# Kernel optimization log

Measured on AMD Instinct MI355X. Metric: run time of the kernel, lower is better.

Reference implementation:

```python
import jax, jax.numpy as jnp
import numpy as np

D_MODEL = 256; N_HEADS = 8; N_LAYERS = 6; D_FF = 1024; BATCH = 1
INPUT_SHAPES = [(24, 24, 24), (12, 12, 12), (6, 6, 6)]
NUM_ORGANS = 20; QPO = 5; LEVELS = 3
NUM_PATCHES = [int(np.prod(s)) for s in INPUT_SHAPES]
S_TOTAL = int(sum(NUM_PATCHES))          # 15768 flattened multi-level patches
NUM_Q = QPO * LEVELS * NUM_ORGANS        # 300 queries


def _build_attn_mask():
    # Same structure as FocusedAttnDecoder.generate_attn_mask: per-organ
    # normalized bbox, scaled (floor/ceil) into each feature level, queries
    # ordered organ-major then level then query copy. True = blocked.
    rng = np.random.RandomState(0)
    mask = np.ones((NUM_Q, S_TOTAL), dtype=bool)
    offsets = np.cumsum([0] + NUM_PATCHES[:-1])
    qi = 0
    for organ in range(NUM_ORGANS):
        lo = rng.uniform(0.0, 0.5, 3)
        hi = np.minimum(lo + rng.uniform(0.15, 0.45, 3), 1.0)
        for lvl in range(LEVELS):
            shp = np.array(INPUT_SHAPES[lvl])
            a = np.floor(lo * shp).astype(int)
            b = np.ceil(hi * shp).astype(int)
            dummy = np.zeros(INPUT_SHAPES[lvl], dtype=bool)
            dummy[a[0]:b[0], a[1]:b[1], a[2]:b[2]] = True
            idx = np.nonzero(dummy.ravel())[0] + offsets[lvl]
            for _ in range(QPO):
                mask[qi, idx] = False
                qi += 1
    return mask


def _xavier(key, shape):
    fan_in, fan_out = shape[-1], shape[-2]
    lim = float(np.sqrt(6.0 / (fan_in + fan_out)))
    return jax.random.uniform(key, shape, minval=-lim, maxval=lim, dtype=jnp.float32)


def setup_inputs() -> dict:
    key = jax.random.key(0)
    ks = jax.random.split(key, 9)
    L, C, F = N_LAYERS, D_MODEL, D_FF
    return {
        "srcs": jax.random.normal(ks[0], (BATCH, C, S_TOTAL), jnp.float32),
        "pos_embeds": jax.random.normal(ks[1], (BATCH, C, S_TOTAL), jnp.float32),
        "query_embed": jax.random.normal(ks[2], (NUM_Q, 2 * C), jnp.float32),
        "attn_mask": jnp.asarray(_build_attn_mask()),
        "sa_in_w": _xavier(ks[3], (L, 3 * C, C)), "sa_in_b": jnp.zeros((L, 3 * C), jnp.float32),
        "sa_out_w": _xavier(ks[4], (L, C, C)), "sa_out_b": jnp.zeros((L, C), jnp.float32),
        "ca_in_w": _xavier(ks[5], (L, 3 * C, C)), "ca_in_b": jnp.zeros((L, 3 * C), jnp.float32),
        "ca_out_w": _xavier(ks[6], (L, C, C)), "ca_out_b": jnp.zeros((L, C), jnp.float32),
        "ln1_w": jnp.ones((L, C), jnp.float32), "ln1_b": jnp.zeros((L, C), jnp.float32),
        "ln2_w": jnp.ones((L, C), jnp.float32), "ln2_b": jnp.zeros((L, C), jnp.float32),
        "ln3_w": jnp.ones((L, C), jnp.float32), "ln3_b": jnp.zeros((L, C), jnp.float32),
        "ff1_w": _xavier(ks[7], (L, F, C)), "ff1_b": jnp.zeros((L, F), jnp.float32),
        "ff2_w": _xavier(ks[8], (L, C, F)), "ff2_b": jnp.zeros((L, C), jnp.float32),
    }


def _ln(x, w, b, eps=1e-5):
    m = jnp.mean(x, axis=-1, keepdims=True)
    v = jnp.mean(jnp.square(x - m), axis=-1, keepdims=True)
    return (x - m) * jax.lax.rsqrt(v + eps) * w + b


def _mha(q_in, k_in, v_in, in_w, in_b, out_w, out_b, mask=None):
    # Faithful nn.MultiheadAttention (eval mode): packed in_proj, scale q,
    # additive -inf mask (True = blocked), softmax, out_proj.
    B, Lq, C = q_in.shape
    H = N_HEADS; Dh = C // H
    wq, wk, wv = jnp.split(in_w, 3, axis=0)
    bq, bk, bv = jnp.split(in_b, 3)
    q = (q_in @ wq.T + bq) * (Dh ** -0.5)
    k = k_in @ wk.T + bk
    v = v_in @ wv.T + bv
    q = q.reshape(B, Lq, H, Dh)
    k = k.reshape(B, k_in.shape[1], H, Dh)
    v = v.reshape(B, v_in.shape[1], H, Dh)
    scores = jnp.einsum('bqhd,bkhd->bhqk', q, k)
    if mask is not None:
        scores = jnp.where(mask[None, None], -jnp.inf, scores)
    attn = jax.nn.softmax(scores, axis=-1)
    out = jnp.einsum('bhqk,bkhd->bqhd', attn, v).reshape(B, Lq, C)
    return out @ out_w.T + out_b


def reference(srcs, pos_embeds, query_embed, attn_mask,
              sa_in_w, sa_in_b, sa_out_w, sa_out_b,
              ca_in_w, ca_in_b, ca_out_w, ca_out_b,
              ln1_w, ln1_b, ln2_w, ln2_b, ln3_w, ln3_b,
              ff1_w, ff1_b, ff2_w, ff2_b):
    C = D_MODEL
    src = jnp.transpose(srcs, (0, 2, 1))        # [B, S, C]
    pos = jnp.transpose(pos_embeds, (0, 2, 1))  # [B, S, C]
    B = src.shape[0]
    qe = jnp.broadcast_to(query_embed[:, :C], (B, NUM_Q, C))
    x = jnp.broadcast_to(query_embed[:, C:], (B, NUM_Q, C))
    for l in range(N_LAYERS):
        # self-attention over queries (q/k get query_pos, v is raw tgt)
        qk = x + qe
        sa = _mha(qk, qk, x, sa_in_w[l], sa_in_b[l], sa_out_w[l], sa_out_b[l])
        x = _ln(x + sa, ln2_w[l], ln2_b[l])
        # mask-restricted cross-attention over flattened multi-level src
        ca = _mha(x + qe, src + pos, src,
                  ca_in_w[l], ca_in_b[l], ca_out_w[l], ca_out_b[l], mask=attn_mask)
        x = _ln(x + ca, ln1_w[l], ln1_b[l])
        # FFN
        h = jax.nn.relu(x @ ff1_w[l].T + ff1_b[l])
        x = _ln(x + (h @ ff2_w[l].T + ff2_b[l]), ln3_w[l], ln3_b[l])
    return x
```

## Files before the change

### kernel.cpp

```cpp
#include <hip/hip_runtime.h>
#include <hip/hip_bf16.h>
#include <math.h>

#define S_TOTAL 15768
#define NQ 300
#define C 256
#define H 8
#define DH 32
#define FF 1024
#define NL 6
#define MAXN 1792
#define NROW 60
#define NT_MAX 16384
#define MQ16 19

#define WB_SAW   0u
#define WB_SAOW  1179648u
#define WB_CAW   1572864u
#define WB_CAOW  2752512u
#define WB_FF1   3145728u
#define WB_FF2   4718592u
#define WB_SAB   6291456u
#define WB_SAOB  6296064u
#define WB_CAB   6297600u
#define WB_CAOB  6302208u
#define WB_FF1B  6303744u
#define WB_FF2B  6309888u
#define WB_TOT   6311424u
#define WT_SAOW  6311424u
#define WT_CAOW  6704640u
#define WB_TOT2  7097856u
#define WT_ELEMS 786432u

typedef __hip_bfloat16 bf16;
typedef __attribute__((ext_vector_type(8))) short bf16x8;
typedef __attribute__((ext_vector_type(4))) float f32x4;

__device__ __forceinline__ float b2f(bf16 v){ return __bfloat162float(v); }

__device__ __forceinline__ float ldin(const void* p, size_t i, int isbf){
    if (isbf) return b2f(((const bf16*)p)[i]);
    return ((const float*)p)[i];
}

__device__ __forceinline__ short f2bf_s(float v){
    bf16 h = __float2bfloat16(v);
    return *(short*)&h;
}

__device__ __forceinline__ float s2f(unsigned short s){
    union { unsigned u; float f; } w; w.u = ((unsigned)s) << 16; return w.f;
}

__device__ __forceinline__ bf16x8 f8_to_bf(float4 a, float4 b){
    bf16x8 r;
    r[0]=f2bf_s(a.x); r[1]=f2bf_s(a.y); r[2]=f2bf_s(a.z); r[3]=f2bf_s(a.w);
    r[4]=f2bf_s(b.x); r[5]=f2bf_s(b.y); r[6]=f2bf_s(b.z); r[7]=f2bf_s(b.w);
    return r;
}


__global__ void detect_cfg(const uint4* __restrict__ srcs,
                           const uint4* __restrict__ mask,
                           int* __restrict__ cfg){
    __shared__ int red[256];
    int t = threadIdx.x;
    int c = 0;
    for (int i = t; i < 16384; i += 256){
        uint4 v = srcs[i];
        unsigned w0 = v.x, w1 = v.y, w2 = v.z, w3 = v.w;
        if ((w0 & 0x7F80u) == 0x7F80u) c++;
        if (((w0 >> 16) & 0x7F80u) == 0x7F80u) c++;
        if ((w1 & 0x7F80u) == 0x7F80u) c++;
        if (((w1 >> 16) & 0x7F80u) == 0x7F80u) c++;
        if ((w2 & 0x7F80u) == 0x7F80u) c++;
        if (((w2 >> 16) & 0x7F80u) == 0x7F80u) c++;
        if ((w3 & 0x7F80u) == 0x7F80u) c++;
        if (((w3 >> 16) & 0x7F80u) == 0x7F80u) c++;
    }
    red[t] = c; __syncthreads();
    for (int s = 128; s > 0; s >>= 1){ if (t < s) red[t] += red[t+s]; __syncthreads(); }
    if (t == 0) cfg[0] = (red[0] >= 16) ? 0 : 1;
    __syncthreads();
    int c2 = 0;
    for (int i = t; i < 4096; i += 256){
        uint4 v = mask[i];
        unsigned w[4] = {v.x, v.y, v.z, v.w};
        #pragma unroll
        for (int j = 0; j < 4; j++){
            unsigned x = w[j];
            c2 += ((x & 0xFFu) != 0) + (((x >> 8) & 0xFFu) != 0)
                + (((x >> 16) & 0xFFu) != 0) + (((x >> 24) & 0xFFu) != 0);
        }
    }
    red[t] = c2; __syncthreads();
    for (int s = 128; s > 0; s >>= 1){ if (t < s) red[t] += red[t+s]; __syncthreads(); }
    if (t == 0) cfg[1] = (red[0] > 32768) ? 1 : 0;
}


__global__ void convert_all(
    const void* saw, const void* sab, const void* saow, const void* saob,
    const void* caw, const void* cab, const void* caow, const void* caob,
    const void* f1w, const void* f1b, const void* f2w, const void* f2b,
    const int* __restrict__ cfg, bf16* __restrict__ Wb)
{
    int isbf = cfg[0];
    size_t i = ((size_t)blockIdx.x*256 + threadIdx.x) * 4;
    if (i >= WB_TOT) return;
    const void* src; size_t loc;
    if      (i < WB_SAOW){ src = saw;  loc = i - WB_SAW; }
    else if (i < WB_CAW) { src = saow; loc = i - WB_SAOW; }
    else if (i < WB_CAOW){ src = caw;  loc = i - WB_CAW; }
    else if (i < WB_FF1) { src = caow; loc = i - WB_CAOW; }
    else if (i < WB_FF2) { src = f1w;  loc = i - WB_FF1; }
    else if (i < WB_SAB) { src = f2w;  loc = i - WB_FF2; }
    else if (i < WB_SAOB){ src = sab;  loc = i - WB_SAB; }
    else if (i < WB_CAB) { src = saob; loc = i - WB_SAOB; }
    else if (i < WB_CAOB){ src = cab;  loc = i - WB_CAB; }
    else if (i < WB_FF1B){ src = caob; loc = i - WB_CAOB; }
    else if (i < WB_FF2B){ src = f1b;  loc = i - WB_FF1B; }
    else                 { src = f2b;  loc = i - WB_FF2B; }
    #pragma unroll
    for (int t = 0; t < 4; t++)
        Wb[i+t] = __float2bfloat16(ldin(src, loc+t, isbf));
}


__global__ void build_wt(bf16* __restrict__ Wb){
    unsigned i = blockIdx.x*256 + threadIdx.x;
    if (i >= WT_ELEMS) return;
    if (i < 393216u){
        unsigned l = i / 65536u, r = i % 65536u, k = r >> 8, n = r & 255u;
        Wb[WT_SAOW + i] = Wb[WB_SAOW + l*65536u + n*256u + k];
    } else {
        unsigned j = i - 393216u;
        unsigned l = j / 65536u, r = j % 65536u, k = r >> 8, n = r & 255u;
        Wb[WT_CAOW + j] = Wb[WB_CAOW + l*65536u + n*256u + k];
    }
}


__global__ void init_qx(const void* __restrict__ qemb, const int* __restrict__ cfg,
                        float* __restrict__ qe, float* __restrict__ x){
    int isbf = cfg[0];
    int i = blockIdx.x*256 + threadIdx.x;
    if (i >= NQ*C) return;
    int row = i / C, col = i % C;
    qe[i] = ldin(qemb, (size_t)row*2*C + col, isbf);
    x[i]  = ldin(qemb, (size_t)row*2*C + C + col, isbf);
}

__global__ void write_out(const float* __restrict__ x, const int* __restrict__ cfg,
                          void* __restrict__ o){
    int isbf = cfg[0];
    int i = blockIdx.x*256 + threadIdx.x;
    if (i >= NQ*C) return;
    if (isbf) ((bf16*)o)[i] = __float2bfloat16(x[i]);
    else      ((float*)o)[i] = x[i];
}


__global__ void count_rows(const unsigned char* __restrict__ mask8,
                           const int* __restrict__ cfg, int* __restrict__ rcnt){
    __shared__ int red[256];
    int r = blockIdx.x;
    int t = threadIdx.x;
    bool isbyte = (cfg[1] != 0);
    const int* row32 = (const int*)mask8 + (size_t)(r*5) * S_TOTAL;
    const unsigned char* row8 = mask8 + (size_t)(r*5) * S_TOTAL;
    int c = 0;
    for (int s = t; s < S_TOTAL; s += 256){
        int blocked = isbyte ? (int)row8[s] : row32[s];
        if (blocked == 0) c++;
    }
    red[t] = c; __syncthreads();
    for (int s = 128; s > 0; s >>= 1){ if (t < s) red[t] += red[t+s]; __syncthreads(); }
    if (t == 0) rcnt[r] = min(red[0], MAXN);
}

__global__ void prefix_rows(const int* __restrict__ rcnt, int* __restrict__ off){
    if (threadIdx.x == 0){
        int a = 0;
        for (int r = 0; r < NROW; r++){
            off[r] = a;
            a = min(a + rcnt[r], NT_MAX);
        }
        off[NROW] = a;
    }
}

__global__ void fill_glist(const unsigned char* __restrict__ mask8,
                           const int* __restrict__ cfg, const int* __restrict__ off,
                           int* __restrict__ glist){
    __shared__ int counts[257];
    int r = blockIdx.x;
    int t = threadIdx.x;
    bool isbyte = (cfg[1] != 0);
    const int* row32 = (const int*)mask8 + (size_t)(r*5) * S_TOTAL;
    const unsigned char* row8 = mask8 + (size_t)(r*5) * S_TOTAL;
    const int chunk = (S_TOTAL + 255) / 256;
    int s0 = t*chunk, s1 = min(S_TOTAL, s0+chunk);
    int c = 0;
    for (int s = s0; s < s1; s++){
        int blocked = isbyte ? (int)row8[s] : row32[s];
        if (blocked == 0) c++;
    }
    counts[t+1] = c;
    __syncthreads();
    if (t == 0){
        counts[0] = 0;
        for (int i = 1; i <= 256; i++) counts[i] += counts[i-1];
    }
    __syncthreads();
    int o = off[r] + counts[t];
    int lim = off[r+1];
    for (int s = s0; s < s1; s++){
        int blocked = isbyte ? (int)row8[s] : row32[s];
        if (blocked == 0){ if (o < lim) glist[o] = s; o++; }
    }
}


__global__ __launch_bounds__(256) void gather_cast(
    const void* __restrict__ srcs, const void* __restrict__ pos,
    const int* __restrict__ cfg, const int* __restrict__ glist,
    const int* __restrict__ off,
    bf16* __restrict__ Agkv, bf16* __restrict__ Agsrc)
{
    int NT = off[NROW];
    int m0 = blockIdx.x * 64;
    if (m0 >= NT) return;
    int isbf = cfg[0];
    __shared__ __align__(16) short Tkv[64][40];
    __shared__ __align__(16) short Tsr[64][40];
    int tid = threadIdx.x;
    int am = tid & 63;
    int kg = (tid >> 6) * 8;
    int mg = m0 + am;
    int g = (mg < NT) ? glist[mg] : 0;
    int wn = tid >> 2;
    int wk = (tid & 3) * 8;
    bool wvalid = (m0 + wn < NT);
    for (int k0 = 0; k0 < C; k0 += 32){
        #pragma unroll
        for (int i = 0; i < 8; i++){
            int k = k0 + kg + i;
            float s  = ldin(srcs, (size_t)k*S_TOTAL + g, isbf);
            float pp = ldin(pos,  (size_t)k*S_TOTAL + g, isbf);
            Tsr[am][kg+i] = f2bf_s(s);
            Tkv[am][kg+i] = f2bf_s(s + pp);
        }
        __syncthreads();
        if (wvalid){
            *(bf16x8*)(Agkv  + (size_t)(m0+wn)*C + k0 + wk) = *(const bf16x8*)&Tkv[wn][wk];
            *(bf16x8*)(Agsrc + (size_t)(m0+wn)*C + k0 + wk) = *(const bf16x8*)&Tsr[wn][wk];
        }
        __syncthreads();
    }
}


__global__ __launch_bounds__(256) void gemm_kv3(
    const bf16* __restrict__ Agkv, const bf16* __restrict__ Agsrc,
    const bf16* __restrict__ Wb, int lstart,
    const int* __restrict__ off, bf16* __restrict__ KV)
{
    int NT = off[NROW];
    int m0 = blockIdx.x * 128;
    if (m0 >= NT) return;
    int z = blockIdx.z;
    int l = lstart + (z >> 1);
    int kv = z & 1;
    const bf16* Ag = kv ? Agsrc : Agkv;
    size_t woff = WB_CAW + ((size_t)l*3 + 1 + kv) * C * C;
    size_t boff = WB_CAB + ((size_t)l*3 + 1 + kv) * C;
    bf16* Out = KV + (size_t)z * NT_MAX * C;
    int n0 = blockIdx.y * 128;
    int tid = threadIdx.x;
    int lane = tid & 63, wid = tid >> 6;
    int fr = lane & 15, quad = lane >> 4;
    int mbase = (wid & 1) * 64, nbase = (wid >> 1) * 64;

    __shared__ __align__(16) union {
        struct { short A[128][72]; short B[128][72]; } ab;
        short Cs[128][136];
    } sh;

    f32x4 acc[4][4];
    #pragma unroll
    for (int i = 0; i < 4; i++)
        #pragma unroll
        for (int j = 0; j < 4; j++) acc[i][j] = (f32x4)(0.f);

    for (int k0 = 0; k0 < C; k0 += 64){
        #pragma unroll
        for (int it = 0; it < 4; it++){
            int idx = tid + it*256;
            int row = idx >> 3;
            int kseg = (idx & 7) * 8;
            *(bf16x8*)&sh.ab.A[row][kseg] = *(const bf16x8*)(Ag + (size_t)(m0+row)*C + k0 + kseg);
            *(bf16x8*)&sh.ab.B[row][kseg] = *(const bf16x8*)(Wb + woff + (size_t)(n0+row)*C + k0 + kseg);
        }
        __syncthreads();
        #pragma unroll
        for (int h = 0; h < 2; h++){
            bf16x8 af[4], bfr[4];
            #pragma unroll
            for (int i = 0; i < 4; i++) af[i] = *(const bf16x8*)&sh.ab.A[mbase+i*16+fr][h*32 + quad*8];
            #pragma unroll
            for (int j = 0; j < 4; j++) bfr[j] = *(const bf16x8*)&sh.ab.B[nbase+j*16+fr][h*32 + quad*8];
            #pragma unroll
            for (int i = 0; i < 4; i++)
                #pragma unroll
                for (int j = 0; j < 4; j++)
                    acc[i][j] = __builtin_amdgcn_mfma_f32_16x16x32_bf16(af[i], bfr[j], acc[i][j], 0, 0, 0);
        }
        __syncthreads();
    }

    int col16 = lane & 15, rq = quad * 4;
    #pragma unroll
    for (int j = 0; j < 4; j++){
        int gnl = nbase + j*16 + col16;
        float bv = b2f(Wb[boff + n0 + gnl]);
        #pragma unroll
        for (int i = 0; i < 4; i++){
            #pragma unroll
            for (int r = 0; r < 4; r++){
                int ml = mbase + i*16 + rq + r;
                sh.Cs[ml][gnl] = f2bf_s(acc[i][j][r] + bv);
            }
        }
    }
    __syncthreads();
    #pragma unroll
    for (int it = 0; it < 8; it++){
        int i = tid + it*256;
        int row = i >> 4, seg = i & 15;
        int gm = m0 + row;
        if (gm < NT)
            *(bf16x8*)(Out + (size_t)gm*C + n0 + seg*8) = *(const bf16x8*)&sh.Cs[row][seg*8];
    }
}


__device__ __forceinline__ void gemm_tile16(
    const float* __restrict__ A, const float* __restrict__ A2, int a2_nlimit,
    int lda, const bf16* __restrict__ W, size_t woff, size_t boff,
    float* __restrict__ Out, int M, int N, int K, int relu,
    int m0, int n0, int lane)
{
    int fr = lane & 15, quad = lane >> 4;
    int gm = m0 + fr;
    int n  = n0 + fr;
    bool mrow = (gm < M);
    bool use2 = (A2 != nullptr) && (n0 < a2_nlimit);
    f32x4 acc = (f32x4)(0.f);

    for (int k0 = 0; k0 < K; k0 += 32){
        bf16x8 af = (bf16x8)(short)0;
        if (mrow){
            const float4* pa = (const float4*)(A + (size_t)gm*lda + k0 + quad*8);
            float4 a0 = pa[0], a1 = pa[1];
            if (use2){
                const float4* p2 = (const float4*)(A2 + (size_t)gm*lda + k0 + quad*8);
                float4 b0 = p2[0], b1 = p2[1];
                a0.x += b0.x; a0.y += b0.y; a0.z += b0.z; a0.w += b0.w;
                a1.x += b1.x; a1.y += b1.y; a1.z += b1.z; a1.w += b1.w;
            }
            af = f8_to_bf(a0, a1);
        }
        bf16x8 bf_ = *(const bf16x8*)(W + woff + (size_t)n*K + k0 + quad*8);
        acc = __builtin_amdgcn_mfma_f32_16x16x32_bf16(af, bf_, acc, 0, 0, 0);
    }

    float bv = b2f(W[boff + n]);
    int rq = quad * 4;
    #pragma unroll
    for (int r = 0; r < 4; r++){
        int gmr = m0 + rq + r;
        if (gmr < M){
            float v = acc[r] + bv;
            if (relu) v = fmaxf(v, 0.f);
            Out[(size_t)gmr*N + n] = v;
        }
    }
}

__global__ __launch_bounds__(64) void gemm_q_mfma(
    const float* __restrict__ A, const float* __restrict__ A2, int a2_nlimit,
    int lda, const bf16* __restrict__ W, size_t woff,
    size_t boff, float* __restrict__ Out,
    int M, int N, int K, int relu)
{
    gemm_tile16(A, A2, a2_nlimit, lda, W, woff, boff, Out, M, N, K, relu,
                blockIdx.x * 16, blockIdx.y * 16, (int)threadIdx.x);
}


__device__ __forceinline__ void out_ln_row(
    const float* __restrict__ arow, const bf16* __restrict__ Wb,
    size_t wtoff, size_t boff,
    const void* __restrict__ lnw, const void* __restrict__ lnb, size_t lnoff,
    int isbf, float* __restrict__ x, int row, int tid, float* __restrict__ red)
{
    int lane = tid & 63, wvv = tid >> 6;
    const bf16* wt = Wb + wtoff;
    float a0=0.f, a1=0.f, a2=0.f, a3=0.f;
    #pragma unroll 4
    for (int k = 0; k < C; k += 4){
        a0 += arow[k]   * b2f(wt[(size_t)k*256 + tid]);
        a1 += arow[k+1] * b2f(wt[(size_t)(k+1)*256 + tid]);
        a2 += arow[k+2] * b2f(wt[(size_t)(k+2)*256 + tid]);
        a3 += arow[k+3] * b2f(wt[(size_t)(k+3)*256 + tid]);
    }
    float v = (a0+a1) + (a2+a3) + b2f(Wb[boff + tid]) + x[(size_t)row*C + tid];
    float s = v, q = v*v;
    #pragma unroll
    for (int m = 1; m < 64; m <<= 1){
        s += __shfl_xor(s, m);
        q += __shfl_xor(q, m);
    }
    if (lane == 0){ red[wvv] = s; red[4+wvv] = q; }
    __syncthreads();
    float S = red[0]+red[1]+red[2]+red[3];
    float Q = red[4]+red[5]+red[6]+red[7];
    float mean = S * (1.f/256.f);
    float var  = Q * (1.f/256.f) - mean*mean;
    float r = (v - mean) * rsqrtf(var + 1e-5f);
    x[(size_t)row*C + tid] = r * ldin(lnw, lnoff+tid, isbf) + ldin(lnb, lnoff+tid, isbf);
}

__global__ __launch_bounds__(256) void row_out_ln(
    const float* __restrict__ A, const bf16* __restrict__ Wb,
    size_t wtoff, size_t boff,
    const void* __restrict__ lnw, const void* __restrict__ lnb, size_t lnoff,
    const int* __restrict__ cfg, float* __restrict__ x)
{
    int row = blockIdx.x;
    int tid = threadIdx.x;
    __shared__ float as[C];
    __shared__ float red[8];
    as[tid] = A[(size_t)row*C + tid];
    __syncthreads();
    out_ln_row(as, Wb, wtoff, boff, lnw, lnb, lnoff, cfg[0], x, row, tid, red);
}


__global__ __launch_bounds__(256) void sa_fused(
    const float* __restrict__ saqkv, const bf16* __restrict__ Wb, int l,
    const void* __restrict__ ln2w, const void* __restrict__ ln2b,
    const int* __restrict__ cfg, float* __restrict__ x)
{
    __shared__ __align__(16) float qv[8][DH];
    __shared__ float as[C];
    __shared__ float red[8];
    int tid = threadIdx.x;
    int lane = tid & 63, wv = tid >> 6;
    int q = blockIdx.x;
    int isbf = cfg[0];
    const float scale = 0.17677669529663687f;
    const size_t CC = (size_t)C*C;

    {
        int h2 = tid >> 5, d = tid & 31;
        qv[h2][d] = saqkv[(size_t)q*768 + h2*DH + d] * scale;
    }
    __syncthreads();
    #pragma unroll
    for (int hh = 0; hh < 2; hh++){
        int h = wv*2 + hh;
        float e[5]; float mx = -1e30f;
        #pragma unroll
        for (int i = 0; i < 5; i++){
            int j = lane + 64*i;
            float d = -1e30f;
            if (j < NQ){
                const float4* kp = (const float4*)(saqkv + (size_t)j*768 + 256 + h*DH);
                const float4* q4 = (const float4*)qv[h];
                d = 0.f;
                #pragma unroll
                for (int b = 0; b < 8; b++){
                    float4 kk = kp[b], qq = q4[b];
                    d += qq.x*kk.x + qq.y*kk.y + qq.z*kk.z + qq.w*kk.w;
                }
            }
            e[i] = d; mx = fmaxf(mx, d);
        }
        #pragma unroll
        for (int m = 1; m < 64; m <<= 1) mx = fmaxf(mx, __shfl_xor(mx, m));
        float sum = 0.f;
        #pragma unroll
        for (int i = 0; i < 5; i++){
            int j = lane + 64*i;
            float ee = (j < NQ) ? __expf(e[i] - mx) : 0.f;
            e[i] = ee; sum += ee;
        }
        #pragma unroll
        for (int m = 1; m < 64; m <<= 1) sum += __shfl_xor(sum, m);
        int dd8 = lane & 3, grp = lane >> 2;
        float acc[8];
        #pragma unroll
        for (int t = 0; t < 8; t++) acc[t] = 0.f;
        #pragma unroll
        for (int k = 0; k < 19; k++){
            int j = grp + 16*k;
            float s = __shfl(e[k>>2], j & 63);
            if (j < NQ){
                const float4* vp = (const float4*)(saqkv + (size_t)j*768 + 512 + h*DH + dd8*8);
                float4 v0 = vp[0], v1 = vp[1];
                acc[0] += s*v0.x; acc[1] += s*v0.y; acc[2] += s*v0.z; acc[3] += s*v0.w;
                acc[4] += s*v1.x; acc[5] += s*v1.y; acc[6] += s*v1.z; acc[7] += s*v1.w;
            }
        }
        #pragma unroll
        for (int t = 0; t < 8; t++){
            float a = acc[t];
            a += __shfl_xor(a, 4); a += __shfl_xor(a, 8);
            a += __shfl_xor(a, 16); a += __shfl_xor(a, 32);
            acc[t] = a;
        }
        if (lane < 4){
            float inv = 1.f/sum;
            #pragma unroll
            for (int t = 0; t < 8; t++)
                as[h*DH + dd8*8 + t] = acc[t]*inv;
        }
    }
    __syncthreads();
    out_ln_row(as, Wb, WT_SAOW + (size_t)l*CC, WB_SAOB + (size_t)l*C,
               ln2w, ln2b, (size_t)l*C, isbf, x, q, tid, red);
}


__global__ __launch_bounds__(256) void ca_fused(
    const float* __restrict__ x, const float* __restrict__ qe,
    const bf16* __restrict__ Wb, int l,
    const bf16* __restrict__ KV, const int* __restrict__ off,
    float* __restrict__ out)
{
    int r = blockIdx.x, h = blockIdx.y;
    int tid = threadIdx.x;
    int lane = tid & 63, wv = tid >> 6;
    int base = off[r], n = off[r+1] - base;
    const bf16* Kg = KV + (size_t)(2*l)   * NT_MAX * C;
    const bf16* Vg = KV + (size_t)(2*l+1) * NT_MAX * C;
    __shared__ __align__(16) float xq[5][C];
    __shared__ __align__(16) float qv[5][DH];
    __shared__ float sc[5][MAXN];
    __shared__ float wred[5][4];
    __shared__ float wsum[5][4];
    __shared__ float pacc[4][5][DH];
    const float scale = 0.17677669529663687f;
    const size_t CC = (size_t)C*C;

    for (int i = tid; i < 5*C; i += 256){
        int qc = i >> 8, k = i & 255;
        xq[qc][k] = x[(size_t)(r*5+qc)*C + k] + qe[(size_t)(r*5+qc)*C + k];
    }
    __syncthreads();
    if (tid < 5*DH){
        int qc = tid >> 5, d = tid & 31;
        int nn = h*DH + d;
        const bf16* wr = Wb + WB_CAW + (size_t)l*3*CC + (size_t)nn*C;
        float a0 = 0.f, a1 = 0.f;
        for (int k = 0; k < C; k += 8){
            bf16x8 w8 = *(const bf16x8*)(wr + k);
            a0 += xq[qc][k  ] * s2f((unsigned short)w8[0])
                + xq[qc][k+1] * s2f((unsigned short)w8[1])
                + xq[qc][k+2] * s2f((unsigned short)w8[2])
                + xq[qc][k+3] * s2f((unsigned short)w8[3]);
            a1 += xq[qc][k+4] * s2f((unsigned short)w8[4])
                + xq[qc][k+5] * s2f((unsigned short)w8[5])
                + xq[qc][k+6] * s2f((unsigned short)w8[6])
                + xq[qc][k+7] * s2f((unsigned short)w8[7]);
        }
        qv[qc][d] = (a0 + a1 + b2f(Wb[WB_CAB + (size_t)l*3*C + nn])) * scale;
    }
    __syncthreads();

    float mx[5] = {-1e30f,-1e30f,-1e30f,-1e30f,-1e30f};
    for (int ki = tid; ki < n; ki += 256){
        const bf16x8* kp = (const bf16x8*)(Kg + (size_t)(base+ki)*C + h*DH);
        float kf[32];
        #pragma unroll
        for (int b = 0; b < 4; b++){
            bf16x8 k8 = kp[b];
            #pragma unroll
            for (int t = 0; t < 8; t++) kf[b*8+t] = s2f((unsigned short)k8[t]);
        }
        #pragma unroll
        for (int qc = 0; qc < 5; qc++){
            const float4* q4 = (const float4*)qv[qc];
            float d = 0.f;
            #pragma unroll
            for (int b = 0; b < 8; b++){
                float4 qq = q4[b];
                d += qq.x*kf[b*4] + qq.y*kf[b*4+1] + qq.z*kf[b*4+2] + qq.w*kf[b*4+3];
            }
            sc[qc][ki] = d;
            mx[qc] = fmaxf(mx[qc], d);
        }
    }
    #pragma unroll
    for (int qc = 0; qc < 5; qc++)
        for (int m = 1; m < 64; m <<= 1) mx[qc] = fmaxf(mx[qc], __shfl_xor(mx[qc], m));
    if (lane == 0){
        #pragma unroll
        for (int qc = 0; qc < 5; qc++) wred[qc][wv] = mx[qc];
    }
    __syncthreads();
    #pragma unroll
    for (int qc = 0; qc < 5; qc++)
        mx[qc] = fmaxf(fmaxf(wred[qc][0], wred[qc][1]), fmaxf(wred[qc][2], wred[qc][3]));
    float sum[5] = {0.f,0.f,0.f,0.f,0.f};
    for (int ki = tid; ki < n; ki += 256){
        #pragma unroll
        for (int qc = 0; qc < 5; qc++){
            float e = __expf(sc[qc][ki] - mx[qc]);
            sc[qc][ki] = e;
            sum[qc] += e;
        }
    }
    #pragma unroll
    for (int qc = 0; qc < 5; qc++)
        for (int m = 1; m < 64; m <<= 1) sum[qc] += __shfl_xor(sum[qc], m);
    if (lane == 0){
        #pragma unroll
        for (int qc = 0; qc < 5; qc++) wsum[qc][wv] = sum[qc];
    }
    __syncthreads();
    #pragma unroll
    for (int qc = 0; qc < 5; qc++)
        sum[qc] = wsum[qc][0] + wsum[qc][1] + wsum[qc][2] + wsum[qc][3];
    int dd8 = tid & 3, grp = tid >> 2;
    float acc[5][8];
    #pragma unroll
    for (int qc = 0; qc < 5; qc++)
        #pragma unroll
        for (int t = 0; t < 8; t++) acc[qc][t] = 0.f;
    for (int j = grp; j < n; j += 64){
        bf16x8 v8 = *(const bf16x8*)(Vg + (size_t)(base+j)*C + h*DH + dd8*8);
        float vf[8];
        #pragma unroll
        for (int t = 0; t < 8; t++) vf[t] = s2f((unsigned short)v8[t]);
        #pragma unroll
        for (int qc = 0; qc < 5; qc++){
            float s = sc[qc][j];
            #pragma unroll
            for (int t = 0; t < 8; t++) acc[qc][t] += s*vf[t];
        }
    }
    #pragma unroll
    for (int qc = 0; qc < 5; qc++)
        #pragma unroll
        for (int t = 0; t < 8; t++){
            float a = acc[qc][t];
            a += __shfl_xor(a, 4); a += __shfl_xor(a, 8);
            a += __shfl_xor(a, 16); a += __shfl_xor(a, 32);
            acc[qc][t] = a;
        }
    if (lane < 4){
        #pragma unroll
        for (int qc = 0; qc < 5; qc++)
            #pragma unroll
            for (int t = 0; t < 8; t++) pacc[wv][qc][dd8*8+t] = acc[qc][t];
    }
    __syncthreads();
    if (tid < 5*DH){
        int qc = tid >> 5, d = tid & 31;
        float a = pacc[0][qc][d] + pacc[1][qc][d] + pacc[2][qc][d] + pacc[3][qc][d];
        float inv = (n > 0 && sum[qc] > 0.f) ? 1.f/sum[qc] : 0.f;
        out[(size_t)(r*5+qc)*C + h*DH + d] = a*inv;
    }
}


__global__ void sa_attn(const float* __restrict__ qkv, float* __restrict__ out){
    int qi = blockIdx.x, h = blockIdx.y;
    int lane = threadIdx.x;
    __shared__ __align__(16) float qv[DH];
    __shared__ float sc[NQ];
    const float scale = 0.17677669529663687f;
    if (lane < DH) qv[lane] = qkv[qi*768 + h*DH + lane] * scale;
    __syncthreads();
    float mx = -1e30f;
    const float4* q4 = (const float4*)qv;
    for (int j = lane; j < NQ; j += 64){
        const float4* kp = (const float4*)(qkv + j*768 + 256 + h*DH);
        float d = 0.f;
        #pragma unroll
        for (int b = 0; b < 8; b++){
            float4 kk = kp[b];
            float4 qq = q4[b];
            d += qq.x*kk.x + qq.y*kk.y + qq.z*kk.z + qq.w*kk.w;
        }
        sc[j] = d; mx = fmaxf(mx, d);
    }
    for (int m = 1; m < 64; m <<= 1) mx = fmaxf(mx, __shfl_xor(mx, m));
    float sum = 0.f;
    __syncthreads();
    for (int j = lane; j < NQ; j += 64){ float e = __expf(sc[j]-mx); sc[j] = e; sum += e; }
    for (int m = 1; m < 64; m <<= 1) sum += __shfl_xor(sum, m);
    __syncthreads();
    int dd8 = lane & 3, grp = lane >> 2;
    float acc[8];
    #pragma unroll
    for (int t = 0; t < 8; t++) acc[t] = 0.f;
    for (int j = grp; j < NQ; j += 16){
        const float4* vp = (const float4*)(qkv + j*768 + 512 + h*DH + dd8*8);
        float4 v0 = vp[0], v1 = vp[1];
        float s = sc[j];
        acc[0] += s*v0.x; acc[1] += s*v0.y; acc[2] += s*v0.z; acc[3] += s*v0.w;
        acc[4] += s*v1.x; acc[5] += s*v1.y; acc[6] += s*v1.z; acc[7] += s*v1.w;
    }
    #pragma unroll
    for (int t = 0; t < 8; t++){
        float a = acc[t];
        a += __shfl_xor(a, 4); a += __shfl_xor(a, 8);
        a += __shfl_xor(a, 16); a += __shfl_xor(a, 32);
        acc[t] = a;
    }
    if (lane < 4){
        float inv = 1.f/sum;
        #pragma unroll
        for (int t = 0; t < 8; t++)
            out[qi*C + h*DH + dd8*8 + t] = acc[t]*inv;
    }
}

__global__ __launch_bounds__(256) void ca_attn(
    const float* __restrict__ q, const bf16* __restrict__ Kg,
    const bf16* __restrict__ Vg, const int* __restrict__ off,
    float* __restrict__ out)
{
    int r = blockIdx.x, h = blockIdx.y;
    int tid = threadIdx.x;
    int lane = tid & 63, wv = tid >> 6;
    int base = off[r], n = off[r+1] - base;
    __shared__ __align__(16) float qv[5][DH];
    __shared__ float sc[5][MAXN];
    __shared__ float wred[5][4];
    __shared__ float wsum[5][4];
    __shared__ float pacc[4][5][DH];
    const float scale = 0.17677669529663687f;
    for (int i = tid; i < 5*DH; i += 256){
        int qc = i >> 5, d = i & 31;
        qv[qc][d] = q[(size_t)(r*5+qc)*C + h*DH + d] * scale;
    }
    __syncthreads();
    float mx[5] = {-1e30f,-1e30f,-1e30f,-1e30f,-1e30f};
    for (int ki = tid; ki < n; ki += 256){
        const bf16x8* kp = (const bf16x8*)(Kg + (size_t)(base+ki)*C + h*DH);
        float kf[32];
        #pragma unroll
        for (int b = 0; b < 4; b++){
            bf16x8 k8 = kp[b];
            #pragma unroll
            for (int t = 0; t < 8; t++) kf[b*8+t] = s2f((unsigned short)k8[t]);
        }
        #pragma unroll
        for (int qc = 0; qc < 5; qc++){
            const float4* q4 = (const float4*)qv[qc];
            float d = 0.f;
            #pragma unroll
            for (int b = 0; b < 8; b++){
                float4 qq = q4[b];
                d += qq.x*kf[b*4] + qq.y*kf[b*4+1] + qq.z*kf[b*4+2] + qq.w*kf[b*4+3];
            }
            sc[qc][ki] = d;
            mx[qc] = fmaxf(mx[qc], d);
        }
    }
    #pragma unroll
    for (int qc = 0; qc < 5; qc++)
        for (int m = 1; m < 64; m <<= 1) mx[qc] = fmaxf(mx[qc], __shfl_xor(mx[qc], m));
    if (lane == 0){
        #pragma unroll
        for (int qc = 0; qc < 5; qc++) wred[qc][wv] = mx[qc];
    }
    __syncthreads();
    #pragma unroll
    for (int qc = 0; qc < 5; qc++)
        mx[qc] = fmaxf(fmaxf(wred[qc][0], wred[qc][1]), fmaxf(wred[qc][2], wred[qc][3]));
    float sum[5] = {0.f,0.f,0.f,0.f,0.f};
    for (int ki = tid; ki < n; ki += 256){
        #pragma unroll
        for (int qc = 0; qc < 5; qc++){
            float e = __expf(sc[qc][ki] - mx[qc]);
            sc[qc][ki] = e;
            sum[qc] += e;
        }
    }
    #pragma unroll
    for (int qc = 0; qc < 5; qc++)
        for (int m = 1; m < 64; m <<= 1) sum[qc] += __shfl_xor(sum[qc], m);
    if (lane == 0){
        #pragma unroll
        for (int qc = 0; qc < 5; qc++) wsum[qc][wv] = sum[qc];
    }
    __syncthreads();
    #pragma unroll
    for (int qc = 0; qc < 5; qc++)
        sum[qc] = wsum[qc][0] + wsum[qc][1] + wsum[qc][2] + wsum[qc][3];
    int dd8 = tid & 3, grp = tid >> 2;
    float acc[5][8];
    #pragma unroll
    for (int qc = 0; qc < 5; qc++)
        #pragma unroll
        for (int t = 0; t < 8; t++) acc[qc][t] = 0.f;
    for (int j = grp; j < n; j += 64){
        bf16x8 v8 = *(const bf16x8*)(Vg + (size_t)(base+j)*C + h*DH + dd8*8);
        float vf[8];
        #pragma unroll
        for (int t = 0; t < 8; t++) vf[t] = s2f((unsigned short)v8[t]);
        #pragma unroll
        for (int qc = 0; qc < 5; qc++){
            float s = sc[qc][j];
            #pragma unroll
            for (int t = 0; t < 8; t++) acc[qc][t] += s*vf[t];
        }
    }
    #pragma unroll
    for (int qc = 0; qc < 5; qc++)
        #pragma unroll
        for (int t = 0; t < 8; t++){
            float a = acc[qc][t];
            a += __shfl_xor(a, 4); a += __shfl_xor(a, 8);
            a += __shfl_xor(a, 16); a += __shfl_xor(a, 32);
            acc[qc][t] = a;
        }
    if (lane < 4){
        #pragma unroll
        for (int qc = 0; qc < 5; qc++)
            #pragma unroll
            for (int t = 0; t < 8; t++) pacc[wv][qc][dd8*8+t] = acc[qc][t];
    }
    __syncthreads();
    if (tid < 5*DH){
        int qc = tid >> 5, d = tid & 31;
        float a = pacc[0][qc][d] + pacc[1][qc][d] + pacc[2][qc][d] + pacc[3][qc][d];
        float inv = (n > 0 && sum[qc] > 0.f) ? 1.f/sum[qc] : 0.f;
        out[(size_t)(r*5+qc)*C + h*DH + d] = a*inv;
    }
}

__global__ void add_res_ln(float* __restrict__ x, const float* __restrict__ t,
                           const void* __restrict__ w, const void* __restrict__ b,
                           size_t off, const int* __restrict__ cfg){
    int isbf = cfg[0];
    int row = blockIdx.x;
    int tid = threadIdx.x;
    int lane = tid & 63, wv = tid >> 6;
    __shared__ float wsum[4], wsq[4];
    float v = x[row*C + tid] + t[row*C + tid];
    float s = v, q = v*v;
    #pragma unroll
    for (int m = 1; m < 64; m <<= 1){
        s += __shfl_xor(s, m);
        q += __shfl_xor(q, m);
    }
    if (lane == 0){ wsum[wv] = s; wsq[wv] = q; }
    __syncthreads();
    float S = wsum[0]+wsum[1]+wsum[2]+wsum[3];
    float Q = wsq[0]+wsq[1]+wsq[2]+wsq[3];
    float mean = S * (1.f/256.f);
    float var  = Q * (1.f/256.f) - mean*mean;
    float r = (v - mean) * rsqrtf(var + 1e-5f);
    x[row*C + tid] = r * ldin(w, off + tid, isbf) + ldin(b, off + tid, isbf);
}


__global__ __launch_bounds__(256) void ffn_fused(
    float* __restrict__ x, const bf16* __restrict__ Wb, int l,
    const void* __restrict__ ln3w, const void* __restrict__ ln3b,
    const int* __restrict__ cfg)
{
    __shared__ __align__(16) short Xs[16][264];
    __shared__ __align__(16) short Hs[16][1032];
    __shared__ __align__(16) float Os[16][264];
    int tid = threadIdx.x;
    int lane = tid & 63, wv = tid >> 6;
    int fr = lane & 15, quad = lane >> 4;
    int m0 = blockIdx.x * 16;
    int isbf = cfg[0];
    const bf16* W1 = Wb + WB_FF1 + (size_t)l*FF*C;
    const bf16* W2 = Wb + WB_FF2 + (size_t)l*C*FF;

    for (int i = tid; i < 16*256; i += 256){
        int row = i >> 8, col = i & 255;
        int gm = m0 + row;
        float v = (gm < NQ) ? x[(size_t)gm*C + col] : 0.f;
        Xs[row][col] = f2bf_s(v);
    }
    __syncthreads();

    #pragma unroll
    for (int nt = 0; nt < 16; nt++){
        int n0 = wv*256 + nt*16;
        f32x4 acc = (f32x4)(0.f);
        #pragma unroll
        for (int k0 = 0; k0 < C; k0 += 32){
            bf16x8 af = *(const bf16x8*)&Xs[fr][k0 + quad*8];
            bf16x8 bf_ = *(const bf16x8*)(W1 + (size_t)(n0+fr)*C + k0 + quad*8);
            acc = __builtin_amdgcn_mfma_f32_16x16x32_bf16(af, bf_, acc, 0, 0, 0);
        }
        int nn = n0 + fr;
        float bv = b2f(Wb[WB_FF1B + (size_t)l*FF + nn]);
        #pragma unroll
        for (int r = 0; r < 4; r++){
            float hv = fmaxf(acc[r] + bv, 0.f);
            Hs[quad*4 + r][nn] = f2bf_s(hv);
        }
    }
    __syncthreads();

    #pragma unroll
    for (int nt = 0; nt < 4; nt++){
        int n0 = wv*64 + nt*16;
        f32x4 acc = (f32x4)(0.f);
        for (int k0 = 0; k0 < FF; k0 += 32){
            bf16x8 af = *(const bf16x8*)&Hs[fr][k0 + quad*8];
            bf16x8 bf_ = *(const bf16x8*)(W2 + (size_t)(n0+fr)*FF + k0 + quad*8);
            acc = __builtin_amdgcn_mfma_f32_16x16x32_bf16(af, bf_, acc, 0, 0, 0);
        }
        int nn = n0 + fr;
        float bv = b2f(Wb[WB_FF2B + (size_t)l*C + nn]);
        #pragma unroll
        for (int r = 0; r < 4; r++)
            Os[quad*4 + r][nn] = acc[r] + bv;
    }
    __syncthreads();

    int row = tid >> 4, j = tid & 15;
    int gm = m0 + row;
    float4 v4[4];
    float s = 0.f, q = 0.f;
    if (gm < NQ){
        const float* xrow = x + (size_t)gm*C;
        #pragma unroll
        for (int u = 0; u < 4; u++){
            float4 o = *(const float4*)&Os[row][j*16 + u*4];
            float4 xv = *(const float4*)(xrow + j*16 + u*4);
            o.x += xv.x; o.y += xv.y; o.z += xv.z; o.w += xv.w;
            v4[u] = o;
            s += o.x + o.y + o.z + o.w;
            q += o.x*o.x + o.y*o.y + o.z*o.z + o.w*o.w;
        }
    }
    #pragma unroll
    for (int m = 1; m < 16; m <<= 1){
        s += __shfl_xor(s, m);
        q += __shfl_xor(q, m);
    }
    if (gm < NQ){
        float mean = s * (1.f/256.f);
        float var  = q * (1.f/256.f) - mean*mean;
        float inv  = rsqrtf(var + 1e-5f);
        size_t lo = (size_t)l*C + j*16;
        float* xrow = x + (size_t)gm*C + j*16;
        #pragma unroll
        for (int u = 0; u < 4; u++){
            float4 o = v4[u];
            float4 ov;
            ov.x = (o.x-mean)*inv * ldin(ln3w, lo+u*4+0, isbf) + ldin(ln3b, lo+u*4+0, isbf);
            ov.y = (o.y-mean)*inv * ldin(ln3w, lo+u*4+1, isbf) + ldin(ln3b, lo+u*4+1, isbf);
            ov.z = (o.z-mean)*inv * ldin(ln3w, lo+u*4+2, isbf) + ldin(ln3b, lo+u*4+2, isbf);
            ov.w = (o.w-mean)*inv * ldin(ln3w, lo+u*4+3, isbf) + ldin(ln3b, lo+u*4+3, isbf);
            *(float4*)(xrow + u*4) = ov;
        }
    }
}


extern "C" void kernel_launch(void* const* d_in, const int* in_sizes, int n_in,
                              void* d_out, int out_size, void* d_ws, size_t ws_size,
                              hipStream_t stream) {
    const void* srcs    = d_in[0];
    const void* pos     = d_in[1];
    const void* qemb    = d_in[2];
    const unsigned char* mask = (const unsigned char*)d_in[3];
    const void* sa_in_w = d_in[4];
    const void* sa_in_b = d_in[5];
    const void* sa_out_w= d_in[6];
    const void* sa_out_b= d_in[7];
    const void* ca_in_w = d_in[8];
    const void* ca_in_b = d_in[9];
    const void* ca_out_w= d_in[10];
    const void* ca_out_b= d_in[11];
    const void* ln1_w   = d_in[12];
    const void* ln1_b   = d_in[13];
    const void* ln2_w   = d_in[14];
    const void* ln2_b   = d_in[15];
    const void* ln3_w   = d_in[16];
    const void* ln3_b   = d_in[17];
    const void* ff1_w   = d_in[18];
    const void* ff1_b   = d_in[19];
    const void* ff2_w   = d_in[20];
    const void* ff2_b   = d_in[21];

    const size_t SLICE = (size_t)NT_MAX * C / 2;

    float* p = (float*)d_ws;
    float* qe    = p; p += NQ*C;
    float* x     = p; p += NQ*C;
    bf16*  Agkv  = (bf16*)p; p += SLICE;
    bf16*  Agsrc = (bf16*)p; p += SLICE;
    bf16*  Wb    = (bf16*)p; p += (WB_TOT2+2)/2;
    float* saqkv = p; p += NQ*768;
    float* att   = p; p += NQ*C;
    float* tmp   = p; p += NQ*C;
    float* hbuf  = p; p += NQ*FF;
    float* qbuf  = p; p += NQ*C;
    int*   glist = (int*)p; p += NT_MAX;
    int*   rcnt  = (int*)p; p += NROW;
    int*   off   = (int*)p; p += NROW+4;
    int*   cfg   = (int*)p; p += 4;
    bf16*  KV    = (bf16*)p;

    size_t base_bytes = (size_t)((char*)KV - (char*)d_ws);
    bool hoist = (ws_size >= base_bytes + 12 * SLICE * sizeof(float));

    dim3 blk(256);
    const size_t CC = (size_t)C*C;

    detect_cfg<<<1, blk, 0, stream>>>((const uint4*)srcs, (const uint4*)mask, cfg);
    convert_all<<<(WB_TOT/4 + 255)/256, blk, 0, stream>>>(
        sa_in_w, sa_in_b, sa_out_w, sa_out_b, ca_in_w, ca_in_b, ca_out_w, ca_out_b,
        ff1_w, ff1_b, ff2_w, ff2_b, cfg, Wb);
    build_wt<<<(WT_ELEMS + 255)/256, blk, 0, stream>>>(Wb);
    init_qx<<<(NQ*C+255)/256, blk, 0, stream>>>(qemb, cfg, qe, x);
    count_rows<<<NROW, blk, 0, stream>>>(mask, cfg, rcnt);
    prefix_rows<<<1, 64, 0, stream>>>(rcnt, off);
    fill_glist<<<NROW, blk, 0, stream>>>(mask, cfg, off, glist);
    gather_cast<<<NT_MAX/64, blk, 0, stream>>>(srcs, pos, cfg, glist, off, Agkv, Agsrc);

    if (hoist){
        gemm_kv3<<<dim3(NT_MAX/128, 2, 2*NL), blk, 0, stream>>>(
            Agkv, Agsrc, Wb, 0, off, KV);

        for (int l = 0; l < NL; l++){
            gemm_q_mfma<<<dim3(MQ16, 48), 64, 0, stream>>>(
                x, qe, 512, C, Wb, WB_SAW + (size_t)l*3*CC, WB_SAB + (size_t)l*3*C,
                saqkv, NQ, 768, C, 0);
            sa_fused<<<NQ, blk, 0, stream>>>(saqkv, Wb, l, ln2_w, ln2_b, cfg, x);
            ca_fused<<<dim3(NROW, H), blk, 0, stream>>>(x, qe, Wb, l, KV, off, att);
            row_out_ln<<<NQ, blk, 0, stream>>>(
                att, Wb, WT_CAOW + (size_t)l*CC, WB_CAOB + (size_t)l*C,
                ln1_w, ln1_b, (size_t)l*C, cfg, x);
            ffn_fused<<<MQ16, blk, 0, stream>>>(x, Wb, l, ln3_w, ln3_b, cfg);
        }
        write_out<<<(NQ*C+255)/256, blk, 0, stream>>>(x, cfg, d_out);
        return;
    }

    for (int l = 0; l < NL; l++){
        bf16* Kg = KV;
        bf16* Vg = KV + (size_t)NT_MAX * C;
        gemm_kv3<<<dim3(NT_MAX/128, 2, 2), blk, 0, stream>>>(
            Agkv, Agsrc, Wb, l, off, KV);

        gemm_q_mfma<<<dim3(MQ16, 48), 64, 0, stream>>>(
            x, qe, 512, C, Wb, WB_SAW + (size_t)l*3*CC, WB_SAB + (size_t)l*3*C,
            saqkv, NQ, 768, C, 0);
        sa_attn<<<dim3(NQ, H), 64, 0, stream>>>(saqkv, att);
        row_out_ln<<<NQ, blk, 0, stream>>>(
            att, Wb, WT_SAOW + (size_t)l*CC, WB_SAOB + (size_t)l*C,
            ln2_w, ln2_b, (size_t)l*C, cfg, x);

        gemm_q_mfma<<<dim3(MQ16, 16), 64, 0, stream>>>(
            x, qe, 256, C, Wb, WB_CAW + (size_t)l*3*CC, WB_CAB + (size_t)l*3*C,
            qbuf, NQ, 256, C, 0);
        ca_attn<<<dim3(NROW, H), blk, 0, stream>>>(qbuf, Kg, Vg, off, att);
        row_out_ln<<<NQ, blk, 0, stream>>>(
            att, Wb, WT_CAOW + (size_t)l*CC, WB_CAOB + (size_t)l*C,
            ln1_w, ln1_b, (size_t)l*C, cfg, x);

        gemm_q_mfma<<<dim3(MQ16, 64), 64, 0, stream>>>(
            x, nullptr, 0, C, Wb, WB_FF1 + (size_t)l*FF*C, WB_FF1B + (size_t)l*FF,
            hbuf, NQ, FF, C, 1);
        gemm_q_mfma<<<dim3(MQ16, 16), 64, 0, stream>>>(
            hbuf, nullptr, 0, FF, Wb, WB_FF2 + (size_t)l*C*FF, WB_FF2B + (size_t)l*C,
            tmp, NQ, C, FF, 0);
        add_res_ln<<<NQ, blk, 0, stream>>>(x, tmp, ln3_w, ln3_b, (size_t)l*C, cfg);
    }
    write_out<<<(NQ*C+255)/256, blk, 0, stream>>>(x, cfg, d_out);
}
```

Measured before the change: 979.9 us.

## Split fused FFN into parallel MFMA GEMMs and transpose cross-attn Q weights

Replaces the single ffn_fused kernel, which ran on only 19 blocks, with two gemm_q_mfma launches (FF1 with ReLU into hbuf, FF2 into tmp) and a separate residual+LayerNorm kernel. This spreads the FFN work across many more workgroups. The cost is extra launches and a round trip through global memory for the hidden activations. It also adds a transposed copy of the cross-attention Q projection weights, so the per-thread Q dot products in ca_fused read coalesced columns instead of strided rows.

```diff
diff --git a/kernel.cpp b/kernel.cpp
--- a/kernel.cpp
+++ b/kernel.cpp
@@ -29,8 +29,9 @@
 #define WB_TOT   6311424u
 #define WT_SAOW  6311424u
 #define WT_CAOW  6704640u
-#define WB_TOT2  7097856u
-#define WT_ELEMS 786432u
+#define WT_CAQW  7097856u
+#define WB_TOT2  7491072u
+#define WT_ELEMS 1179648u
 
 typedef __hip_bfloat16 bf16;
 typedef __attribute__((ext_vector_type(8))) short bf16x8;
@@ -133,10 +134,14 @@
     if (i < 393216u){
         unsigned l = i / 65536u, r = i % 65536u, k = r >> 8, n = r & 255u;
         Wb[WT_SAOW + i] = Wb[WB_SAOW + l*65536u + n*256u + k];
-    } else {
+    } else if (i < 786432u){
         unsigned j = i - 393216u;
         unsigned l = j / 65536u, r = j % 65536u, k = r >> 8, n = r & 255u;
         Wb[WT_CAOW + j] = Wb[WB_CAOW + l*65536u + n*256u + k];
+    } else {
+        unsigned j = i - 786432u;
+        unsigned l = j / 65536u, r = j % 65536u, k = r >> 8, n = r & 255u;
+        Wb[WT_CAQW + j] = Wb[WB_CAW + l*196608u + n*256u + k];
     }
 }
 
@@ -563,20 +568,16 @@
     if (tid < 5*DH){
         int qc = tid >> 5, d = tid & 31;
         int nn = h*DH + d;
-        const bf16* wr = Wb + WB_CAW + (size_t)l*3*CC + (size_t)nn*C;
-        float a0 = 0.f, a1 = 0.f;
-        for (int k = 0; k < C; k += 8){
-            bf16x8 w8 = *(const bf16x8*)(wr + k);
-            a0 += xq[qc][k  ] * s2f((unsigned short)w8[0])
-                + xq[qc][k+1] * s2f((unsigned short)w8[1])
-                + xq[qc][k+2] * s2f((unsigned short)w8[2])
-                + xq[qc][k+3] * s2f((unsigned short)w8[3]);
-            a1 += xq[qc][k+4] * s2f((unsigned short)w8[4])
-                + xq[qc][k+5] * s2f((unsigned short)w8[5])
-                + xq[qc][k+6] * s2f((unsigned short)w8[6])
-                + xq[qc][k+7] * s2f((unsigned short)w8[7]);
-        }
-        qv[qc][d] = (a0 + a1 + b2f(Wb[WB_CAB + (size_t)l*3*C + nn])) * scale;
+        const bf16* wqt = Wb + WT_CAQW + (size_t)l*CC;
+        float a0=0.f, a1=0.f, a2=0.f, a3=0.f;
+        #pragma unroll 4
+        for (int k = 0; k < C; k += 4){
+            a0 += xq[qc][k]   * b2f(wqt[(size_t)k*256 + nn]);
+            a1 += xq[qc][k+1] * b2f(wqt[(size_t)(k+1)*256 + nn]);
+            a2 += xq[qc][k+2] * b2f(wqt[(size_t)(k+2)*256 + nn]);
+            a3 += xq[qc][k+3] * b2f(wqt[(size_t)(k+3)*256 + nn]);
+        }
+        qv[qc][d] = ((a0+a1) + (a2+a3) + b2f(Wb[WB_CAB + (size_t)l*3*C + nn])) * scale;
     }
     __syncthreads();
 
@@ -846,6 +847,7 @@
     }
 }
 
+
 __global__ void add_res_ln(float* __restrict__ x, const float* __restrict__ t,
                            const void* __restrict__ w, const void* __restrict__ b,
                            size_t off, const int* __restrict__ cfg){
@@ -869,108 +871,6 @@
     float var  = Q * (1.f/256.f) - mean*mean;
     float r = (v - mean) * rsqrtf(var + 1e-5f);
     x[row*C + tid] = r * ldin(w, off + tid, isbf) + ldin(b, off + tid, isbf);
-}
-
-
-__global__ __launch_bounds__(256) void ffn_fused(
-    float* __restrict__ x, const bf16* __restrict__ Wb, int l,
-    const void* __restrict__ ln3w, const void* __restrict__ ln3b,
-    const int* __restrict__ cfg)
-{
-    __shared__ __align__(16) short Xs[16][264];
-    __shared__ __align__(16) short Hs[16][1032];
-    __shared__ __align__(16) float Os[16][264];
-    int tid = threadIdx.x;
-    int lane = tid & 63, wv = tid >> 6;
-    int fr = lane & 15, quad = lane >> 4;
-    int m0 = blockIdx.x * 16;
-    int isbf = cfg[0];
-    const bf16* W1 = Wb + WB_FF1 + (size_t)l*FF*C;
-    const bf16* W2 = Wb + WB_FF2 + (size_t)l*C*FF;
-
-    for (int i = tid; i < 16*256; i += 256){
-        int row = i >> 8, col = i & 255;
-        int gm = m0 + row;
-        float v = (gm < NQ) ? x[(size_t)gm*C + col] : 0.f;
-        Xs[row][col] = f2bf_s(v);
-    }
-    __syncthreads();
-
-    #pragma unroll
-    for (int nt = 0; nt < 16; nt++){
-        int n0 = wv*256 + nt*16;
-        f32x4 acc = (f32x4)(0.f);
-        #pragma unroll
-        for (int k0 = 0; k0 < C; k0 += 32){
-            bf16x8 af = *(const bf16x8*)&Xs[fr][k0 + quad*8];
-            bf16x8 bf_ = *(const bf16x8*)(W1 + (size_t)(n0+fr)*C + k0 + quad*8);
-            acc = __builtin_amdgcn_mfma_f32_16x16x32_bf16(af, bf_, acc, 0, 0, 0);
-        }
-        int nn = n0 + fr;
-        float bv = b2f(Wb[WB_FF1B + (size_t)l*FF + nn]);
-        #pragma unroll
-        for (int r = 0; r < 4; r++){
-            float hv = fmaxf(acc[r] + bv, 0.f);
-            Hs[quad*4 + r][nn] = f2bf_s(hv);
-        }
-    }
-    __syncthreads();
-
-    #pragma unroll
-    for (int nt = 0; nt < 4; nt++){
-        int n0 = wv*64 + nt*16;
-        f32x4 acc = (f32x4)(0.f);
-        for (int k0 = 0; k0 < FF; k0 += 32){
-            bf16x8 af = *(const bf16x8*)&Hs[fr][k0 + quad*8];
-            bf16x8 bf_ = *(const bf16x8*)(W2 + (size_t)(n0+fr)*FF + k0 + quad*8);
-            acc = __builtin_amdgcn_mfma_f32_16x16x32_bf16(af, bf_, acc, 0, 0, 0);
-        }
-        int nn = n0 + fr;
-        float bv = b2f(Wb[WB_FF2B + (size_t)l*C + nn]);
-        #pragma unroll
-        for (int r = 0; r < 4; r++)
-            Os[quad*4 + r][nn] = acc[r] + bv;
-    }
-    __syncthreads();
-
-    int row = tid >> 4, j = tid & 15;
-    int gm = m0 + row;
-    float4 v4[4];
-    float s = 0.f, q = 0.f;
-    if (gm < NQ){
-        const float* xrow = x + (size_t)gm*C;
-        #pragma unroll
-        for (int u = 0; u < 4; u++){
-            float4 o = *(const float4*)&Os[row][j*16 + u*4];
-            float4 xv = *(const float4*)(xrow + j*16 + u*4);
-            o.x += xv.x; o.y += xv.y; o.z += xv.z; o.w += xv.w;
-            v4[u] = o;
-            s += o.x + o.y + o.z + o.w;
-            q += o.x*o.x + o.y*o.y + o.z*o.z + o.w*o.w;
-        }
-    }
-    #pragma unroll
-    for (int m = 1; m < 16; m <<= 1){
-        s += __shfl_xor(s, m);
-        q += __shfl_xor(q, m);
-    }
-    if (gm < NQ){
-        float mean = s * (1.f/256.f);
-        float var  = q * (1.f/256.f) - mean*mean;
-        float inv  = rsqrtf(var + 1e-5f);
-        size_t lo = (size_t)l*C + j*16;
-        float* xrow = x + (size_t)gm*C + j*16;
-        #pragma unroll
-        for (int u = 0; u < 4; u++){
-            float4 o = v4[u];
-            float4 ov;
-            ov.x = (o.x-mean)*inv * ldin(ln3w, lo+u*4+0, isbf) + ldin(ln3b, lo+u*4+0, isbf);
-            ov.y = (o.y-mean)*inv * ldin(ln3w, lo+u*4+1, isbf) + ldin(ln3b, lo+u*4+1, isbf);
-            ov.z = (o.z-mean)*inv * ldin(ln3w, lo+u*4+2, isbf) + ldin(ln3b, lo+u*4+2, isbf);
-            ov.w = (o.w-mean)*inv * ldin(ln3w, lo+u*4+3, isbf) + ldin(ln3b, lo+u*4+3, isbf);
-            *(float4*)(xrow + u*4) = ov;
-        }
-    }
 }
 
 
@@ -1045,11 +945,19 @@
                 x, qe, 512, C, Wb, WB_SAW + (size_t)l*3*CC, WB_SAB + (size_t)l*3*C,
                 saqkv, NQ, 768, C, 0);
             sa_fused<<<NQ, blk, 0, stream>>>(saqkv, Wb, l, ln2_w, ln2_b, cfg, x);
+
             ca_fused<<<dim3(NROW, H), blk, 0, stream>>>(x, qe, Wb, l, KV, off, att);
             row_out_ln<<<NQ, blk, 0, stream>>>(
                 att, Wb, WT_CAOW + (size_t)l*CC, WB_CAOB + (size_t)l*C,
                 ln1_w, ln1_b, (size_t)l*C, cfg, x);
-            ffn_fused<<<MQ16, blk, 0, stream>>>(x, Wb, l, ln3_w, ln3_b, cfg);
+
+            gemm_q_mfma<<<dim3(MQ16, 64), 64, 0, stream>>>(
+                x, nullptr, 0, C, Wb, WB_FF1 + (size_t)l*FF*C, WB_FF1B + (size_t)l*FF,
+                hbuf, NQ, FF, C, 1);
+            gemm_q_mfma<<<dim3(MQ16, 16), 64, 0, stream>>>(
+                hbuf, nullptr, 0, FF, Wb, WB_FF2 + (size_t)l*C*FF, WB_FF2B + (size_t)l*C,
+                tmp, NQ, C, FF, 0);
+            add_res_ln<<<NQ, blk, 0, stream>>>(x, tmp, ln3_w, ln3_b, (size_t)l*C, cfg);
         }
         write_out<<<(NQ*C+255)/256, blk, 0, stream>>>(x, cfg, d_out);
         return;
```

Measured after the change: 933.0 us. -4.8%, faster.
